# Optimization experiments

Measured on AMD Instinct MI355X. Metric: run time of the kernel, lower is better.

## Reference

```python
import jax, jax.numpy as jnp
import numpy as np

VOCAB, D = 50000, 300
B, LC = 64, 32
T, LT = 256, 64
N_SENTS = 5


def setup_inputs() -> dict:
    key = jax.random.key(0)
    k1, k2, k3 = jax.random.split(key, 3)
    claim = jax.random.randint(k1, (B, LC), 0, VOCAB)
    targets = jax.random.randint(k2, (B, T, LT), 0, VOCAB)
    embeddings = jax.random.normal(k3, (VOCAB, D), dtype=jnp.float32)
    return {"claim": claim, "targets": targets, "embeddings": embeddings, "n": N_SENTS}


def reference(claim, targets, embeddings, n):
    # Embedding lookups (frozen table)
    c = embeddings[claim]          # [B, Lc, d]
    t = embeddings[targets]        # [B, T, Lt, d]
    # batch_U = claim[:,None] @ targets^T  -> [B, T, Lc, Lt]
    U = jnp.einsum('bcd,btld->btcl', c, t)
    # softmax over target tokens (axis=3), max over claim tokens (axis=2)
    sm = jax.nn.softmax(U, axis=3)
    scores = jnp.max(sm, axis=2)           # [B, T, Lt]
    target_scores = jnp.sum(scores, axis=2)  # [B, T]
    # per-batch top-n target sentences (sorted order; torch used sorted=False,
    # the selected set is identical)
    _, idx = jax.lax.top_k(target_scores, n)  # [B, n]
    top = jnp.take_along_axis(U, idx[:, :, None, None], axis=1)  # [B, n, Lc, Lt]
    # L2-normalize over last axis (torch dim=2 of the [n, Lc, Lt] slice)
    norm = jnp.sqrt(jnp.sum(top * top, axis=3, keepdims=True))
    return top / norm
```

## Files before the change

### kernel.cpp

```cpp
#include <hip/hip_runtime.h>

#define VOCAB 50000
#define D     300
#define B_    64
#define LC    32
#define T_    256
#define LT    64
#define NSEL  5
#define NCAND 16

#define A_U4   2560
#define A_HALF 20480
#define TROW   320

typedef _Float16 half8_t __attribute__((ext_vector_type(8)));
typedef float    f32x4   __attribute__((ext_vector_type(4)));


__global__ __launch_bounds__(256) void k_prep(const int* __restrict__ claim,
                                              const float* __restrict__ emb,
                                              _Float16* __restrict__ tab,
                                              _Float16* __restrict__ wsA,
                                              int tableBlocks) {
    int wave = threadIdx.x >> 6, lane = threadIdx.x & 63;
    if ((int)blockIdx.x < tableBlocks) {
        int r = blockIdx.x * 4 + wave;
        const float* src = emb + (size_t)r * D;
        _Float16* d = tab + (size_t)r * TROW;
#pragma unroll
        for (int i = 0; i < 5; ++i) {
            int k = lane + i * 64;
            d[k] = (k < D) ? (_Float16)src[k] : (_Float16)0.0f;
        }
    } else {
        int row = (blockIdx.x - tableBlocks) * 4 + wave;
        int b = row >> 5, m = row & 31;
        int tok = claim[row];
        const float* src = emb + (size_t)tok * D;
        _Float16* base = wsA + (size_t)b * A_HALF;
#pragma unroll
        for (int i = 0; i < 5; ++i) {
            int k = lane + i * 64;
            float x = (k < D) ? src[k] : 0.0f;
            _Float16 h = (_Float16)x;
            int sp = ((k >> 3) ^ (m & 7));
            int idx = (m * 40 + sp) * 8 + (k & 7);
            base[idx] = h;
            base[10240 + idx] = (_Float16)(x - (float)h);
        }
    }
}

__device__ __forceinline__ void split8(const float4& a, const float4& b,
                                       half8_t& hv, half8_t& lv) {
    float x[8] = {a.x, a.y, a.z, a.w, b.x, b.y, b.z, b.w};
#pragma unroll
    for (int i = 0; i < 8; ++i) {
        _Float16 h = (_Float16)x[i];
        hv[i] = h;
        lv[i] = (_Float16)(x[i] - (float)h);
    }
}

template<int NI>
__device__ __forceinline__ void compute_exact(const uint4* sA,
                                              const float* __restrict__ emb,
                                              const int* __restrict__ trow, int lcol0,
                                              int lane, f32x4 acc[2][NI]) {
    int ln = lane & 15, quad = lane >> 4;
#pragma unroll
    for (int mi = 0; mi < 2; ++mi)
#pragma unroll
        for (int ni = 0; ni < NI; ++ni) acc[mi][ni] = (f32x4)0.0f;

    int arow0 = ln * 40;
    int arow1 = (16 + ln) * 40;
    int key = ln & 7;
    int qo = quad * 8;

    const float* bp[NI];
#pragma unroll
    for (int ni = 0; ni < NI; ++ni) {
        int tok = trow[lcol0 + ni * 16 + ln];
        bp[ni] = emb + (size_t)tok * D;
    }
#pragma unroll 1
    for (int ks = 0; ks < 10; ++ks) {
        int kb = ks * 32 + qo;
        int ka = kb > 296 ? 296 : kb;
        int kb4 = kb + 4;
        int kbb = kb4 > 296 ? 296 : kb4;
        float4 b0[NI], b1[NI];
#pragma unroll
        for (int ni = 0; ni < NI; ++ni) {
            b0[ni] = *(const float4*)(bp[ni] + ka);
            b1[ni] = *(const float4*)(bp[ni] + kbb);
        }
        if (kb >= 296) {
            float4 z = make_float4(0.f, 0.f, 0.f, 0.f);
#pragma unroll
            for (int ni = 0; ni < NI; ++ni) {
                if (kb >= 300) b0[ni] = z;
                b1[ni] = z;
            }
        }
        int sp = (ks * 4 + quad) ^ key;
        half8_t ah[2], al[2];
        ah[0] = __builtin_bit_cast(half8_t, sA[arow0 + sp]);
        al[0] = __builtin_bit_cast(half8_t, sA[1280 + arow0 + sp]);
        ah[1] = __builtin_bit_cast(half8_t, sA[arow1 + sp]);
        al[1] = __builtin_bit_cast(half8_t, sA[1280 + arow1 + sp]);
        half8_t bh[NI], bl[NI];
#pragma unroll
        for (int ni = 0; ni < NI; ++ni) split8(b0[ni], b1[ni], bh[ni], bl[ni]);
#pragma unroll
        for (int mi = 0; mi < 2; ++mi)
#pragma unroll
            for (int ni = 0; ni < NI; ++ni) {
                acc[mi][ni] = __builtin_amdgcn_mfma_f32_16x16x32_f16(ah[mi], bh[ni], acc[mi][ni], 0, 0, 0);
                acc[mi][ni] = __builtin_amdgcn_mfma_f32_16x16x32_f16(ah[mi], bl[ni], acc[mi][ni], 0, 0, 0);
                acc[mi][ni] = __builtin_amdgcn_mfma_f32_16x16x32_f16(al[mi], bh[ni], acc[mi][ni], 0, 0, 0);
            }
    }
}

__device__ __forceinline__ void compute_noisy(const uint4* sA,
                                              const _Float16* __restrict__ tab,
                                              const int* __restrict__ trow,
                                              int lane, f32x4 acc[2][4]) {
    int ln = lane & 15, quad = lane >> 4;
#pragma unroll
    for (int mi = 0; mi < 2; ++mi)
#pragma unroll
        for (int ni = 0; ni < 4; ++ni) acc[mi][ni] = (f32x4)0.0f;

    int arow0 = ln * 40;
    int arow1 = (16 + ln) * 40;
    int key = ln & 7;
    int qo = quad * 8;

    const _Float16* rp[4];
#pragma unroll
    for (int ni = 0; ni < 4; ++ni) {
        int tok = trow[ni * 16 + ln];
        rp[ni] = tab + (size_t)tok * TROW;
    }
    half8_t bh[2][4];
#pragma unroll
    for (int ni = 0; ni < 4; ++ni) bh[0][ni] = *(const half8_t*)(rp[ni] + qo);
#pragma unroll
    for (int ks = 0; ks < 10; ++ks) {
        int cur = ks & 1, nxt = cur ^ 1;
        if (ks < 9) {
            int ko = (ks + 1) * 32 + qo;
#pragma unroll
            for (int ni = 0; ni < 4; ++ni)
                bh[nxt][ni] = *(const half8_t*)(rp[ni] + ko);
        }
        int sp = (ks * 4 + quad) ^ key;
        half8_t ah[2], al[2];
        ah[0] = __builtin_bit_cast(half8_t, sA[arow0 + sp]);
        al[0] = __builtin_bit_cast(half8_t, sA[1280 + arow0 + sp]);
        ah[1] = __builtin_bit_cast(half8_t, sA[arow1 + sp]);
        al[1] = __builtin_bit_cast(half8_t, sA[1280 + arow1 + sp]);
#pragma unroll
        for (int mi = 0; mi < 2; ++mi)
#pragma unroll
            for (int ni = 0; ni < 4; ++ni) {
                acc[mi][ni] = __builtin_amdgcn_mfma_f32_16x16x32_f16(ah[mi], bh[cur][ni], acc[mi][ni], 0, 0, 0);
                acc[mi][ni] = __builtin_amdgcn_mfma_f32_16x16x32_f16(al[mi], bh[cur][ni], acc[mi][ni], 0, 0, 0);
            }
    }
}

__device__ __forceinline__ float xmax4(float v) {
    v = fmaxf(v, __shfl_xor(v, 1)); v = fmaxf(v, __shfl_xor(v, 2));
    v = fmaxf(v, __shfl_xor(v, 4)); v = fmaxf(v, __shfl_xor(v, 8));
    return v;
}
__device__ __forceinline__ float xsum4(float v) {
    v += __shfl_xor(v, 1); v += __shfl_xor(v, 2);
    v += __shfl_xor(v, 4); v += __shfl_xor(v, 8);
    return v;
}

__device__ __forceinline__ float score_from_acc(f32x4 acc[2][4]) {
    float score_l[4] = {0.f, 0.f, 0.f, 0.f};
#pragma unroll
    for (int mi = 0; mi < 2; ++mi)
#pragma unroll
        for (int r = 0; r < 4; ++r) {
            float m = fmaxf(fmaxf(acc[mi][0][r], acc[mi][1][r]),
                            fmaxf(acc[mi][2][r], acc[mi][3][r]));
            m = xmax4(m);
            float p[4], s = 0.f;
#pragma unroll
            for (int ni = 0; ni < 4; ++ni) { p[ni] = __expf(acc[mi][ni][r] - m); s += p[ni]; }
            s = xsum4(s);
            float rv = 1.0f / s;
#pragma unroll
            for (int ni = 0; ni < 4; ++ni) score_l[ni] = fmaxf(score_l[ni], p[ni] * rv);
        }
    float tot = 0.f;
#pragma unroll
    for (int ni = 0; ni < 4; ++ni) {
        float v = score_l[ni];
        v = fmaxf(v, __shfl_xor(v, 16));
        v = fmaxf(v, __shfl_xor(v, 32));
        tot += v;
    }
    return xsum4(tot);
}

template<bool FAST>
__global__ __launch_bounds__(256, 4) void k_scores(const int* __restrict__ targets,
                                                   const float* __restrict__ emb,
                                                   const _Float16* __restrict__ tab,
                                                   const _Float16* __restrict__ wsA,
                                                   float* __restrict__ wsScr) {
    __shared__ __align__(16) uint4 sA[A_U4];
    int wg = blockIdx.x;
    int xcd = wg & 7, rest = wg >> 3;
    int b = xcd * 8 + (rest >> 6);
    int tg = rest & 63;
    int tid = threadIdx.x;
    {
        const uint4* src = (const uint4*)(wsA + (size_t)b * A_HALF);
        for (int i = tid; i < A_U4; i += 256) sA[i] = src[i];
    }
    __syncthreads();

    int lane = tid & 63, wave = tid >> 6;
    int t = tg * 4 + wave;
    const int* trow = targets + ((size_t)b * T_ + t) * LT;

    f32x4 acc[2][4];
    if (FAST) compute_noisy(sA, tab, trow, lane, acc);
    else      compute_exact<4>(sA, emb, trow, 0, lane, acc);
    float tot = score_from_acc(acc);
    if (lane == 0) wsScr[b * T_ + t] = tot;
}

__global__ __launch_bounds__(256) void k_sel(const int* __restrict__ targets,
                                             const float* __restrict__ emb,
                                             const _Float16* __restrict__ wsA,
                                             const float* __restrict__ wsScr,
                                             int* __restrict__ wsIdx) {
    __shared__ __align__(16) uint4 sA[A_U4];
    __shared__ int sCand[NCAND];
    __shared__ float sScore[NCAND];
    int b = blockIdx.x, tid = threadIdx.x;
    int lane = tid & 63, wave = tid >> 6;
    {
        const uint4* src = (const uint4*)(wsA + (size_t)b * A_HALF);
        for (int i = tid; i < A_U4; i += 256) sA[i] = src[i];
    }
    if (wave == 0) {
        float v[4];
#pragma unroll
        for (int i = 0; i < 4; ++i) v[i] = wsScr[b * T_ + lane + 64 * i];
        for (int r = 0; r < NCAND; ++r) {
            float bv = v[0]; int bi = lane;
#pragma unroll
            for (int i = 1; i < 4; ++i) {
                int idx = lane + 64 * i;
                if (v[i] > bv) { bv = v[i]; bi = idx; }
            }
            for (int off = 32; off > 0; off >>= 1) {
                float ov = __shfl_down(bv, off);
                int   oi = __shfl_down(bi, off);
                if (ov > bv || (ov == bv && oi < bi)) { bv = ov; bi = oi; }
            }
            bi = __shfl(bi, 0);
            if (lane == 0) sCand[r] = bi;
            if ((bi & 63) == lane) v[bi >> 6] = -1e30f;
        }
    }
    __syncthreads();

    for (int r = 0; r < NCAND / 4; ++r) {
        int t = sCand[r * 4 + wave];
        const int* trow = targets + ((size_t)b * T_ + t) * LT;
        f32x4 acc[2][4];
        compute_exact<4>(sA, emb, trow, 0, lane, acc);
        float tot = score_from_acc(acc);
        if (lane == 0) sScore[r * 4 + wave] = tot;
    }
    __syncthreads();

    if (tid == 0) {
        unsigned used = 0;
        for (int j = 0; j < NSEL; ++j) {
            float bs = -1e30f; int bt = 0x7fffffff, bsl = 0;
            for (int s = 0; s < NCAND; ++s) {
                if (used & (1u << s)) continue;
                float sc = sScore[s]; int tt = sCand[s];
                if (sc > bs || (sc == bs && tt < bt)) { bs = sc; bt = tt; bsl = s; }
            }
            used |= (1u << bsl);
            wsIdx[b * NSEL + j] = bt;
        }
    }
}

__global__ __launch_bounds__(256) void k_output(const int* __restrict__ targets,
                                                const float* __restrict__ emb,
                                                const _Float16* __restrict__ wsA,
                                                const int* __restrict__ wsIdx,
                                                float* __restrict__ out) {
    __shared__ __align__(16) uint4 sA[A_U4];
    __shared__ float sS[LC][4];
    int b = blockIdx.y, j = blockIdx.x, tid = threadIdx.x;
    int lane = tid & 63, wave = tid >> 6;
    {
        const uint4* src = (const uint4*)(wsA + (size_t)b * A_HALF);
        for (int i = tid; i < A_U4; i += 256) sA[i] = src[i];
    }
    __syncthreads();

    int t = wsIdx[b * NSEL + j];
    const int* trow = targets + ((size_t)b * T_ + t) * LT;
    f32x4 acc[2][1];
    compute_exact<1>(sA, emb, trow, wave * 16, lane, acc);

    int ln = lane & 15, quad = lane >> 4;
#pragma unroll
    for (int mi = 0; mi < 2; ++mi)
#pragma unroll
        for (int r = 0; r < 4; ++r) {
            float v = acc[mi][0][r] * acc[mi][0][r];
            v = xsum4(v);
            if (ln == 0) sS[mi * 16 + quad * 4 + r][wave] = v;
        }
    __syncthreads();

    float* obase = out + (size_t)(b * NSEL + j) * (LC * LT);
#pragma unroll
    for (int mi = 0; mi < 2; ++mi)
#pragma unroll
        for (int r = 0; r < 4; ++r) {
            int c = mi * 16 + quad * 4 + r;
            float ss = sS[c][0] + sS[c][1] + sS[c][2] + sS[c][3];
            float rinv = 1.0f / sqrtf(ss);
            obase[c * LT + wave * 16 + ln] = acc[mi][0][r] * rinv;
        }
}

extern "C" void kernel_launch(void* const* d_in, const int* in_sizes, int n_in,
                              void* d_out, int out_size, void* d_ws, size_t ws_size,
                              hipStream_t stream) {
    const int*   claim   = (const int*)d_in[0];
    const int*   targets = (const int*)d_in[1];
    const float* emb     = (const float*)d_in[2];

    const size_t tabBytes = (size_t)VOCAB * TROW * sizeof(_Float16);
    const size_t restBytes = (size_t)B_ * A_HALF * sizeof(_Float16)
                           + (size_t)B_ * T_ * sizeof(float)
                           + (size_t)B_ * NSEL * sizeof(int) + 256;
    bool fast = ws_size >= tabBytes + restBytes;

    char* p = (char*)d_ws;
    _Float16* tab = nullptr;
    if (fast) { tab = (_Float16*)p; p += tabBytes; }
    _Float16* wsA = (_Float16*)p; p += (size_t)B_ * A_HALF * sizeof(_Float16);
    float* wsScr = (float*)p;     p += (size_t)B_ * T_ * sizeof(float);
    int*   wsIdx = (int*)p;
    float* out   = (float*)d_out;

    int tableBlocks = fast ? (VOCAB / 4) : 0;
    k_prep<<<dim3(tableBlocks + 512), dim3(256), 0, stream>>>(claim, emb, tab, wsA, tableBlocks);
    if (fast) {
        k_scores<true><<<dim3(B_ * 64), dim3(256), 0, stream>>>(targets, emb, tab, wsA, wsScr);
    } else {
        k_scores<false><<<dim3(B_ * 64), dim3(256), 0, stream>>>(targets, emb, tab, wsA, wsScr);
    }
    k_sel<<<dim3(B_), dim3(256), 0, stream>>>(targets, emb, wsA, wsScr, wsIdx);
    k_output<<<dim3(NSEL, B_), dim3(256), 0, stream>>>(targets, emb, wsA, wsIdx, out);
}
```

Before: 266.5 us.

## Split candidate rescoring across blocks and move final top-n selection into output kernel

The candidate-rescoring stage previously used one block per batch, and each block looped over 16 candidates serially. It now launches 4 blocks per batch, each rescoring 4 candidates exactly, and writes the candidate ids and scores to workspace. The final top-5 pick moves into k_output: lane 0 of wave 0 redoes the selection while the other waves load the claim tile into shared memory. This raises parallelism on a small grid of 64 blocks and overlaps the loads with the selection, at the cost of the top-16 selection being repeated per block.

```diff
diff --git a/kernel.cpp b/kernel.cpp
--- a/kernel.cpp
+++ b/kernel.cpp
@@ -245,21 +245,20 @@
                                              const float* __restrict__ emb,
                                              const _Float16* __restrict__ wsA,
                                              const float* __restrict__ wsScr,
-                                             int* __restrict__ wsIdx) {
+                                             int* __restrict__ wsCand,
+                                             float* __restrict__ wsScoreC) {
     __shared__ __align__(16) uint4 sA[A_U4];
     __shared__ int sCand[NCAND];
-    __shared__ float sScore[NCAND];
-    int b = blockIdx.x, tid = threadIdx.x;
+    int r = blockIdx.x, b = blockIdx.y, tid = threadIdx.x;
     int lane = tid & 63, wave = tid >> 6;
-    {
+    if (wave) {
         const uint4* src = (const uint4*)(wsA + (size_t)b * A_HALF);
-        for (int i = tid; i < A_U4; i += 256) sA[i] = src[i];
-    }
-    if (wave == 0) {
+        for (int i = tid - 64; i < A_U4; i += 192) sA[i] = src[i];
+    } else {
         float v[4];
 #pragma unroll
         for (int i = 0; i < 4; ++i) v[i] = wsScr[b * T_ + lane + 64 * i];
-        for (int r = 0; r < NCAND; ++r) {
+        for (int s = 0; s < NCAND; ++s) {
             float bv = v[0]; int bi = lane;
 #pragma unroll
             for (int i = 1; i < 4; ++i) {
@@ -272,53 +271,56 @@
                 if (ov > bv || (ov == bv && oi < bi)) { bv = ov; bi = oi; }
             }
             bi = __shfl(bi, 0);
-            if (lane == 0) sCand[r] = bi;
+            if (lane == 0) {
+                sCand[s] = bi;
+                if (r == 0) wsCand[b * NCAND + s] = bi;
+            }
             if ((bi & 63) == lane) v[bi >> 6] = -1e30f;
         }
     }
     __syncthreads();
 
-    for (int r = 0; r < NCAND / 4; ++r) {
-        int t = sCand[r * 4 + wave];
-        const int* trow = targets + ((size_t)b * T_ + t) * LT;
-        f32x4 acc[2][4];
-        compute_exact<4>(sA, emb, trow, 0, lane, acc);
-        float tot = score_from_acc(acc);
-        if (lane == 0) sScore[r * 4 + wave] = tot;
-    }
-    __syncthreads();
-
-    if (tid == 0) {
-        unsigned used = 0;
-        for (int j = 0; j < NSEL; ++j) {
+    int c = r * 4 + wave;
+    int t = sCand[c];
+    const int* trow = targets + ((size_t)b * T_ + t) * LT;
+    f32x4 acc[2][4];
+    compute_exact<4>(sA, emb, trow, 0, lane, acc);
+    float tot = score_from_acc(acc);
+    if (lane == 0) wsScoreC[b * NCAND + c] = tot;
+}
+
+__global__ __launch_bounds__(256) void k_output(const int* __restrict__ targets,
+                                                const float* __restrict__ emb,
+                                                const _Float16* __restrict__ wsA,
+                                                const int* __restrict__ wsCand,
+                                                const float* __restrict__ wsScoreC,
+                                                float* __restrict__ out) {
+    __shared__ __align__(16) uint4 sA[A_U4];
+    __shared__ float sS[LC][4];
+    __shared__ int sT;
+    int b = blockIdx.y, j = blockIdx.x, tid = threadIdx.x;
+    int lane = tid & 63, wave = tid >> 6;
+    if (wave) {
+        const uint4* src = (const uint4*)(wsA + (size_t)b * A_HALF);
+        for (int i = tid - 64; i < A_U4; i += 192) sA[i] = src[i];
+    } else if (lane == 0) {
+        unsigned used = 0; int sel = 0;
+        for (int jj = 0; jj <= j; ++jj) {
             float bs = -1e30f; int bt = 0x7fffffff, bsl = 0;
             for (int s = 0; s < NCAND; ++s) {
                 if (used & (1u << s)) continue;
-                float sc = sScore[s]; int tt = sCand[s];
+                float sc = wsScoreC[b * NCAND + s];
+                int tt = wsCand[b * NCAND + s];
                 if (sc > bs || (sc == bs && tt < bt)) { bs = sc; bt = tt; bsl = s; }
             }
             used |= (1u << bsl);
-            wsIdx[b * NSEL + j] = bt;
-        }
-    }
-}
-
-__global__ __launch_bounds__(256) void k_output(const int* __restrict__ targets,
-                                                const float* __restrict__ emb,
-                                                const _Float16* __restrict__ wsA,
-                                                const int* __restrict__ wsIdx,
-                                                float* __restrict__ out) {
-    __shared__ __align__(16) uint4 sA[A_U4];
-    __shared__ float sS[LC][4];
-    int b = blockIdx.y, j = blockIdx.x, tid = threadIdx.x;
-    int lane = tid & 63, wave = tid >> 6;
-    {
-        const uint4* src = (const uint4*)(wsA + (size_t)b * A_HALF);
-        for (int i = tid; i < A_U4; i += 256) sA[i] = src[i];
+            sel = bt;
+        }
+        sT = sel;
     }
     __syncthreads();
 
-    int t = wsIdx[b * NSEL + j];
+    int t = sT;
     const int* trow = targets + ((size_t)b * T_ + t) * LT;
     f32x4 acc[2][1];
     compute_exact<1>(sA, emb, trow, wave * 16, lane, acc);
@@ -356,7 +358,7 @@
     const size_t tabBytes = (size_t)VOCAB * TROW * sizeof(_Float16);
     const size_t restBytes = (size_t)B_ * A_HALF * sizeof(_Float16)
                            + (size_t)B_ * T_ * sizeof(float)
-                           + (size_t)B_ * NSEL * sizeof(int) + 256;
+                           + (size_t)B_ * NCAND * (sizeof(int) + sizeof(float)) + 256;
     bool fast = ws_size >= tabBytes + restBytes;
 
     char* p = (char*)d_ws;
@@ -364,7 +366,8 @@
     if (fast) { tab = (_Float16*)p; p += tabBytes; }
     _Float16* wsA = (_Float16*)p; p += (size_t)B_ * A_HALF * sizeof(_Float16);
     float* wsScr = (float*)p;     p += (size_t)B_ * T_ * sizeof(float);
-    int*   wsIdx = (int*)p;
+    int*   wsCand = (int*)p;      p += (size_t)B_ * NCAND * sizeof(int);
+    float* wsScoreC = (float*)p;
     float* out   = (float*)d_out;
 
     int tableBlocks = fast ? (VOCAB / 4) : 0;
@@ -374,6 +377,6 @@
     } else {
         k_scores<false><<<dim3(B_ * 64), dim3(256), 0, stream>>>(targets, emb, tab, wsA, wsScr);
     }
-    k_sel<<<dim3(B_), dim3(256), 0, stream>>>(targets, emb, wsA, wsScr, wsIdx);
-    k_output<<<dim3(NSEL, B_), dim3(256), 0, stream>>>(targets, emb, wsA, wsIdx, out);
-}
+    k_sel<<<dim3(NCAND / 4, B_), dim3(256), 0, stream>>>(targets, emb, wsA, wsScr, wsCand, wsScoreC);
+    k_output<<<dim3(NSEL, B_), dim3(256), 0, stream>>>(targets, emb, wsA, wsCand, wsScoreC, out);
+}
```

New measurement: 235.2 us. 11.7% less time.
